# Optimization experiments

Hardware: AMD Instinct MI355X
Metric: run time of the kernel (lower is better)

Reference implementation:

```python
import jax, jax.numpy as jnp
import numpy as np

PRE_NMS_TOP_N = 1024
POST_NMS_TOP_N = 256
NMS_THRESH = 0.7
MIN_SIZE = 4.0
SCORE_THRESH = 0.1
BASE_SIZE = 1024.0
SCALE = 0.25            # feature stride = 1/SCALE = 4
IMG_H, IMG_W = 1024.0, 1024.0
NEG_INF = -1e30
CAP = 8                 # max vertices of 4-gon intersect 4-gon


def setup_inputs() -> dict:
    key = jax.random.key(0)
    k1, k2 = jax.random.split(key)
    N, A, H, W = 2, 1, 256, 256
    objectness = jax.random.normal(k1, (N, A, H, W), dtype=jnp.float32)
    box_regression = jax.random.uniform(k2, (N, A * 5, H, W), dtype=jnp.float32) * 0.05
    return {"objectness": objectness, "box_regression": box_regression}


def eastbox2rbox(reg, H, W):
    # reg: (H*W, 5) -> rotated boxes (H*W, 5) in xywha (angle in degrees)
    jy, jx = jnp.meshgrid(jnp.arange(H, dtype=reg.dtype), jnp.arange(W, dtype=reg.dtype), indexing="ij")
    cx0 = (jx / SCALE).reshape(-1)
    cy0 = (jy / SCALE).reshape(-1)
    t = reg[:, 0] * BASE_SIZE
    r = reg[:, 1] * BASE_SIZE
    b = reg[:, 2] * BASE_SIZE
    l = reg[:, 3] * BASE_SIZE
    ang = (reg[:, 4] - 0.5) * 90.0
    w = l + r
    h = t + b
    xc = cx0 + 0.5 * (r - l)
    yc = cy0 + 0.5 * (b - t)
    return jnp.stack([xc, yc, w, h, ang], axis=-1)


def rbox_corners(box):
    # box: (5,) xywha -> (4,2) CCW corners
    th = box[4] * (jnp.pi / 180.0)
    c, s = jnp.cos(th), jnp.sin(th)
    dx = jnp.array([-0.5, 0.5, 0.5, -0.5], box.dtype) * box[2]
    dy = jnp.array([-0.5, -0.5, 0.5, 0.5], box.dtype) * box[3]
    return jnp.stack([box[0] + dx * c - dy * s, box[1] + dx * s + dy * c], axis=-1)


def clip_halfplane(poly, n, p1, p2):
    # Sutherland-Hodgman clip of a convex polygon (CAP,2) with n valid verts
    # against the half-plane left of directed edge p1->p2.
    M = poly.shape[0]
    idx = jnp.arange(M)
    valid = idx < n
    nxt = poly[jnp.where(idx + 1 < n, idx + 1, 0)]
    e = p2 - p1
    d_cur = e[0] * (poly[:, 1] - p1[1]) - e[1] * (poly[:, 0] - p1[0])
    d_nxt = e[0] * (nxt[:, 1] - p1[1]) - e[1] * (nxt[:, 0] - p1[0])
    in_cur = d_cur >= 0.0
    in_nxt = d_nxt >= 0.0
    denom = d_cur - d_nxt
    safe = jnp.where(jnp.abs(denom) > 1e-9, denom, 1.0)
    t = d_cur / safe
    inter = poly + t[:, None] * (nxt - poly)
    emit_cur = in_cur & valid
    emit_int = (in_cur != in_nxt) & valid
    pts = jnp.stack([poly, inter], axis=1).reshape(2 * M, 2)
    flags = jnp.stack([emit_cur, emit_int], axis=1).reshape(2 * M)
    pos = jnp.where(flags, jnp.cumsum(flags) - 1, M)  # M = dropped
    out = jnp.zeros((M, 2), poly.dtype).at[pos].set(jnp.where(flags[:, None], pts, 0.0), mode="drop")
    return out, jnp.sum(flags)


def intersect_area(pa, pb):
    # area of convex intersection of two 4-gons (each (4,2), CCW)
    poly = jnp.zeros((CAP, 2), pa.dtype).at[:4].set(pa)
    n = jnp.asarray(4, jnp.int32)
    for k in range(4):
        poly, n = clip_halfplane(poly, n, pb[k], pb[(k + 1) % 4])
    idx = jnp.arange(CAP)
    valid = idx < n
    nxt = poly[jnp.where(idx + 1 < n, idx + 1, 0)]
    cr = poly[:, 0] * nxt[:, 1] - nxt[:, 0] * poly[:, 1]
    area = 0.5 * jnp.abs(jnp.sum(jnp.where(valid, cr, 0.0)))
    return jnp.where(n >= 3, area, 0.0)


def riou(a, b):
    inter = intersect_area(rbox_corners(a), rbox_corners(b))
    union = a[2] * a[3] + b[2] * b[3] - inter
    return inter / jnp.maximum(union, 1e-9)


def greedy_nms(iou_mat, valid, thresh):
    K = valid.shape[0]
    ar = jnp.arange(K)

    def body(i, state):
        keep, sup = state
        is_keep = valid[i] & jnp.logical_not(sup[i])
        keep = keep.at[i].set(is_keep)
        sup = sup | (is_keep & (iou_mat[i] > thresh) & (ar > i))
        return keep, sup

    keep, _ = jax.lax.fori_loop(0, K, body, (jnp.zeros(K, bool), jnp.zeros(K, bool)))
    return keep


def process_image(obj, reg):
    A, H, W = obj.shape
    scores = obj.transpose(1, 2, 0).reshape(-1)       # (H*W*A,)
    reg5 = reg[:5].transpose(1, 2, 0).reshape(-1, 5)  # (H*W, 5)
    rboxes = eastbox2rbox(reg5, H, W)
    top_scores, top_idx = jax.lax.top_k(scores, PRE_NMS_TOP_N)
    boxes = rboxes[top_idx]
    valid = top_scores > SCORE_THRESH                 # eval-mode score thresh (masked, not dropped)
    # clip_to_image: clamp rotated-box centers into the image
    boxes = boxes.at[:, 0].set(jnp.clip(boxes[:, 0], 0.0, IMG_W - 1.0))
    boxes = boxes.at[:, 1].set(jnp.clip(boxes[:, 1], 0.0, IMG_H - 1.0))
    # remove_small_boxes
    valid = valid & (boxes[:, 2] >= MIN_SIZE) & (boxes[:, 3] >= MIN_SIZE)
    # full rotated IoU matrix, row-by-row to bound memory
    iou_mat = jax.lax.map(lambda a: jax.vmap(lambda b: riou(a, b))(boxes), boxes)
    keep = greedy_nms(iou_mat, valid, NMS_THRESH)
    sel = jnp.where(keep, top_scores, NEG_INF)
    fin_scores, fin_idx = jax.lax.top_k(sel, POST_NMS_TOP_N)
    fin_boxes = boxes[fin_idx]
    fin_valid = keep[fin_idx]
    out = jnp.concatenate([fin_boxes, fin_scores[:, None]], axis=-1)  # (post, 6) = xywha + score
    return jnp.where(fin_valid[:, None], out, 0.0)


def reference(objectness, box_regression):
    return jax.vmap(process_image)(objectness, box_regression)
```

## Files before the change

kernel.cpp:

```cpp
#include <hip/hip_runtime.h>
#include <hip/hip_bf16.h>

#define N_IMG 2
#define HW 65536
#define PRE 1024
#define POST 256
#define NBIN 4096
#define SORTN 4096
#define PAIRCAP 131072
#define NMS_THR 0.7f
#define SCORE_T 0.1f
#define MIN_SZ 4.0f

__device__ __forceinline__ unsigned int fkey(float f) {
    unsigned int u = __float_as_uint(f);
    return u ^ ((u & 0x80000000u) ? 0xFFFFFFFFu : 0x80000000u);
}
__device__ __forceinline__ float unfkey(unsigned int k) {
    unsigned int u = (k & 0x80000000u) ? (k ^ 0x80000000u) : ~k;
    return __uint_as_float(u);
}
__device__ __forceinline__ unsigned long long readlane64(unsigned long long v, int l) {
    unsigned int lo = (unsigned int)__builtin_amdgcn_readlane((int)(unsigned int)v, l);
    unsigned int hi = (unsigned int)__builtin_amdgcn_readlane((int)(unsigned int)(v >> 32), l);
    return ((unsigned long long)hi << 32) | (unsigned long long)lo;
}

__global__ void k_init(unsigned long long* masks, unsigned int* hist, unsigned int* cnts) {
    int t = blockIdx.x * blockDim.x + threadIdx.x;
    if (t < N_IMG * PRE * 16) masks[t] = 0ULL;
    if (t < N_IMG * NBIN) hist[t] = 0u;
    if (t < 8) cnts[t] = 0u;
}

__global__ __launch_bounds__(1024) void k_hista(const float* __restrict__ obj,
                                                unsigned int* hist) {
    __shared__ unsigned int lh[NBIN];
    int img = blockIdx.x >> 3;
    int seg = blockIdx.x & 7;
    for (int i = threadIdx.x; i < NBIN; i += 1024) lh[i] = 0u;
    __syncthreads();
    const float4* o4 = (const float4*)(obj + (size_t)img * HW);
    int base = seg * 2048;
#pragma unroll
    for (int k = 0; k < 2; ++k) {
        float4 v = o4[base + threadIdx.x + k * 1024];
        atomicAdd(&lh[fkey(v.x) >> 20], 1u);
        atomicAdd(&lh[fkey(v.y) >> 20], 1u);
        atomicAdd(&lh[fkey(v.z) >> 20], 1u);
        atomicAdd(&lh[fkey(v.w) >> 20], 1u);
    }
    __syncthreads();
    for (int i = threadIdx.x; i < NBIN; i += 1024) {
        unsigned int c = lh[i];
        if (c) atomicAdd(&hist[img * NBIN + i], c);
    }
}

__global__ void k_findbin(const unsigned int* __restrict__ hist, unsigned int* selB) {
    __shared__ unsigned int lh[NBIN];
    __shared__ unsigned int chunk[256];
    int img = blockIdx.x;
    int t = threadIdx.x;
    unsigned int s = 0;
    for (int k = 0; k < 16; ++k) {
        unsigned int v = hist[img * NBIN + t * 16 + k];
        lh[t * 16 + k] = v;
        s += v;
    }
    chunk[t] = s;
    __syncthreads();
    if (t == 0) {
        unsigned int run = 0;
        int c;
        for (c = 255; c >= 0; --c) {
            if (run + chunk[c] >= PRE) break;
            run += chunk[c];
        }
        unsigned int B = 0;
        for (int b = c * 16 + 15; b >= c * 16; --b) {
            if (run + lh[b] >= PRE) { B = (unsigned int)b; break; }
            run += lh[b];
        }
        selB[img] = B;
    }
}

__global__ __launch_bounds__(256) void k_compact(const float* __restrict__ obj,
                                                 const unsigned int* __restrict__ selB,
                                                 unsigned int* cnts, unsigned long long* cbuf) {
    __shared__ unsigned long long lbuf[1024];
    __shared__ unsigned int lcnt, lbase;
    int t = blockIdx.x * 256 + threadIdx.x;
    const float4* o4 = (const float4*)obj;
#pragma unroll
    for (int k = 0; k < 2; ++k) {
        if (threadIdx.x == 0) lcnt = 0;
        __syncthreads();
        int p = t + k * 16384;
        int img = p >> 14;
        unsigned int B = selB[img];
        float4 v = o4[p];
        float vs[4] = {v.x, v.y, v.z, v.w};
#pragma unroll
        for (int c = 0; c < 4; ++c) {
            unsigned int key = fkey(vs[c]);
            if ((key >> 20) >= B) {
                unsigned int i = (unsigned int)((p & 16383) * 4 + c);
                unsigned int pos = atomicAdd(&lcnt, 1u);
                lbuf[pos] = ((unsigned long long)key << 32) |
                            (unsigned long long)(0xFFFFFFFFu - i);
            }
        }
        __syncthreads();
        if (threadIdx.x == 0) lbase = atomicAdd(&cnts[img], lcnt);
        __syncthreads();
        unsigned int n = lcnt, base = lbase;
        for (unsigned int q = threadIdx.x; q < n; q += 256) {
            unsigned int gp = base + q;
            if (gp < SORTN) cbuf[img * SORTN + gp] = lbuf[q];
        }
        __syncthreads();
    }
}

__global__ __launch_bounds__(256) void k_rank(const unsigned int* __restrict__ cnts,
                                              const unsigned long long* __restrict__ cbuf,
                                              unsigned long long* sorted) {
    __shared__ unsigned long long keys[SORTN];
    int img = blockIdx.x >> 4;
    int slice = blockIdx.x & 15;
    unsigned int M = cnts[img]; if (M > SORTN) M = SORTN;
    for (unsigned int i = threadIdx.x; i < M; i += 256) keys[i] = cbuf[img * SORTN + i];
    __syncthreads();
    unsigned int cid = (unsigned int)slice * 256 + threadIdx.x;
    if (cid < M) {
        unsigned long long c = keys[cid];
        unsigned int r = 0;
        for (unsigned int j = 0; j < M; ++j) r += (keys[j] > c) ? 1u : 0u;
        if (r < PRE) sorted[img * PRE + r] = c;
    }
}

__global__ __launch_bounds__(128) void k_decode(const unsigned long long* __restrict__ sorted,
                                                const float* __restrict__ boxreg,
                                                float* boxes, float* corn, float4* circ,
                                                unsigned long long* vmask, float* tscr) {
    int g = blockIdx.x * 128 + threadIdx.x;
    int img = g >> 10;
    int t = g & 1023;
    unsigned long long v = sorted[g];
    unsigned int key = (unsigned int)(v >> 32);
    unsigned int idx = (0xFFFFFFFFu - (unsigned int)(v & 0xFFFFFFFFULL)) & 0xFFFFu;
    float sc = unfkey(key);
    int h = (int)(idx >> 8);
    int w = (int)(idx & 255u);
    const float* rg = boxreg + (size_t)img * 5 * HW;
    float t_ = rg[0 * HW + idx] * 1024.0f;
    float rr = rg[1 * HW + idx] * 1024.0f;
    float bb = rg[2 * HW + idx] * 1024.0f;
    float ll = rg[3 * HW + idx] * 1024.0f;
    float ang = (rg[4 * HW + idx] - 0.5f) * 90.0f;
    float wd = ll + rr;
    float ht = t_ + bb;
    float xc = (float)w * 4.0f + 0.5f * (rr - ll);
    float yc = (float)h * 4.0f + 0.5f * (bb - t_);
    xc = fminf(fmaxf(xc, 0.0f), 1023.0f);
    yc = fminf(fmaxf(yc, 0.0f), 1023.0f);
    bool valid = (sc > SCORE_T) && (wd >= MIN_SZ) && (ht >= MIN_SZ);

    float* bx = boxes + (size_t)g * 5;
    bx[0] = xc; bx[1] = yc; bx[2] = wd; bx[3] = ht; bx[4] = ang;
    tscr[g] = sc;

    float th = ang * (float)(3.14159265358979323846 / 180.0);
    float c = cosf(th), s = sinf(th);
    const float dxs[4] = {-0.5f, 0.5f, 0.5f, -0.5f};
    const float dys[4] = {-0.5f, -0.5f, 0.5f, 0.5f};
    float* cr = corn + (size_t)g * 8;
#pragma unroll
    for (int k = 0; k < 4; ++k) {
        float dx = dxs[k] * wd, dy = dys[k] * ht;
        cr[2 * k]     = xc + dx * c - dy * s;
        cr[2 * k + 1] = yc + dx * s + dy * c;
    }
    circ[g] = make_float4(xc, yc, 0.5f * sqrtf(wd * wd + ht * ht) + 0.01f, wd * ht);

    unsigned long long bal = __ballot(valid ? 1 : 0);
    if ((t & 63) == 0) vmask[img * 16 + (t >> 6)] = bal;
}

__global__ __launch_bounds__(256) void k_pairs(const float4* __restrict__ circ,
                                               unsigned int* cnts, unsigned int* pairs) {
    __shared__ unsigned int lbuf[1024];
    __shared__ unsigned int lcnt, lbase;
    if (threadIdx.x == 0) lcnt = 0;
    __syncthreads();
    int t0 = blockIdx.x * 256 + threadIdx.x;
#pragma unroll
    for (int k = 0; k < 16; ++k) {
        int p = t0 + k * 131072;
        int img = p >> 20;
        int r = p & 1048575;
        int i = r >> 10, j = r & 1023;
        if (j > i) {
            float4 a = circ[img * PRE + i];
            float4 b = circ[img * PRE + j];
            float dx = b.x - a.x, dy = b.y - a.y, rr = a.z + b.z;
            if (dx * dx + dy * dy <= rr * rr) {
                unsigned int pr = ((unsigned int)img << 20) | ((unsigned int)i << 10) | (unsigned int)j;
                unsigned int pos = atomicAdd(&lcnt, 1u);
                if (pos < 1024) lbuf[pos] = pr;
                else {
                    unsigned int gp = atomicAdd(&cnts[2], 1u);
                    if (gp < PAIRCAP) pairs[gp] = pr;
                }
            }
        }
    }
    __syncthreads();
    unsigned int n = lcnt; if (n > 1024) n = 1024;
    if (threadIdx.x == 0) lbase = atomicAdd(&cnts[2], n);
    __syncthreads();
    unsigned int base = lbase;
    for (unsigned int q = threadIdx.x; q < n; q += 256) {
        unsigned int gp = base + q;
        if (gp < PAIRCAP) pairs[gp] = lbuf[q];
    }
}

__global__ __launch_bounds__(256) void k_clip(const unsigned int* __restrict__ cnts,
                                              const unsigned int* __restrict__ pairs,
                                              const float* __restrict__ corn,
                                              const float4* __restrict__ circ,
                                              unsigned long long* masks) {
    __shared__ float SPX[8][256], SPY[8][256], SQX[8][256], SQY[8][256];
    int tid = threadIdx.x;
    unsigned int total = cnts[2]; if (total > PAIRCAP) total = PAIRCAP;
    for (unsigned int p = blockIdx.x * 256 + tid; p < total; p += 128 * 256) {
        unsigned int pr = pairs[p];
        int img = (int)(pr >> 20);
        int i = (int)((pr >> 10) & 1023);
        int j = (int)(pr & 1023);
        int ra = img * PRE + i, rb = img * PRE + j;
        const float4* ca = (const float4*)(corn + (size_t)ra * 8);
        float4 a0 = ca[0], a1 = ca[1];
        const float4* cb = (const float4*)(corn + (size_t)rb * 8);
        float4 b0 = cb[0], b1 = cb[1];
        float cbx[4] = {b0.x, b0.z, b1.x, b1.z};
        float cby[4] = {b0.y, b0.w, b1.y, b1.w};
        SPX[0][tid] = a0.x; SPY[0][tid] = a0.y;
        SPX[1][tid] = a0.z; SPY[1][tid] = a0.w;
        SPX[2][tid] = a1.x; SPY[2][tid] = a1.y;
        SPX[3][tid] = a1.z; SPY[3][tid] = a1.w;
        int n = 4;
#pragma unroll
        for (int e = 0; e < 4; ++e) {
            float (*PX)[256] = (e & 1) ? SQX : SPX;
            float (*PY)[256] = (e & 1) ? SQY : SPY;
            float (*QX)[256] = (e & 1) ? SPX : SQX;
            float (*QY)[256] = (e & 1) ? SPY : SQY;
            float p1x = cbx[e], p1y = cby[e];
            int e2 = (e + 1) & 3;
            float ex = cbx[e2] - p1x, ey = cby[e2] - p1y;
            int m = 0;
            for (int k = 0; k < n; ++k) {
                int kn = (k + 1 < n) ? k + 1 : 0;
                float cx_ = PX[k][tid], cy_ = PY[k][tid];
                float nx_ = PX[kn][tid], ny_ = PY[kn][tid];
                float dc = ex * (cy_ - p1y) - ey * (cx_ - p1x);
                float dn = ex * (ny_ - p1y) - ey * (nx_ - p1x);
                bool ic = dc >= 0.0f;
                bool inx = dn >= 0.0f;
                if (ic && m < 8) { QX[m][tid] = cx_; QY[m][tid] = cy_; ++m; }
                if ((ic != inx) && m < 8) {
                    float den = dc - dn;
                    float safe = (fabsf(den) > 1e-9f) ? den : 1.0f;
                    float tt = dc / safe;
                    QX[m][tid] = cx_ + tt * (nx_ - cx_);
                    QY[m][tid] = cy_ + tt * (ny_ - cy_);
                    ++m;
                }
            }
            n = m;
        }
        float inter = 0.0f;
        if (n >= 3) {
            float s = 0.0f;
            for (int k = 0; k < n; ++k) {
                int kn = (k + 1 < n) ? k + 1 : 0;
                s += SPX[k][tid] * SPY[kn][tid] - SPX[kn][tid] * SPY[k][tid];
            }
            inter = 0.5f * fabsf(s);
        }
        float uni = circ[ra].w + circ[rb].w - inter;
        float iou = inter / fmaxf(uni, 1e-9f);
        if (iou > NMS_THR)
            atomicOr(&masks[(size_t)ra * 16 + (j >> 6)], 1ULL << (j & 63));
    }
}

__global__ __launch_bounds__(1024) void k_nms_out(const unsigned long long* __restrict__ masks,
                                                  const unsigned long long* __restrict__ vmask,
                                                  const float* __restrict__ boxes,
                                                  const float* __restrict__ tscr,
                                                  float* __restrict__ out) {
    __shared__ unsigned long long lm[PRE * 16];
    __shared__ unsigned short keptIdx[POST];
    __shared__ int sTotal;
    int img = blockIdx.x;
    int t = threadIdx.x;
    const unsigned long long* mbase = masks + (size_t)img * PRE * 16;
    {
        const ulonglong2* src = (const ulonglong2*)mbase;
        ulonglong2* dst = (ulonglong2*)lm;
#pragma unroll
        for (int k = 0; k < 8; ++k) dst[t + k * 1024] = src[t + k * 1024];
    }
    __syncthreads();

    if (t < 64) {
        int lane = t;
        int lw = lane & 15;
        unsigned long long vmw = vmask[img * 16 + lw];
        unsigned long long supw = 0ULL;
        int cnt = 0;
        for (int b = 0; b < 16 && cnt < POST; ++b) {
            unsigned long long avail = readlane64(vmw, b) & ~readlane64(supw, b);
            while (avail && cnt < POST) {
                unsigned long long a = avail;
                int d0 = __ffsll((long long)a) - 1; a &= a - 1;
                int d1 = a ? __ffsll((long long)a) - 1 : 64; a &= a - 1;
                int d2 = a ? __ffsll((long long)a) - 1 : 64; a &= a - 1;
                int d3 = a ? __ffsll((long long)a) - 1 : 64; a &= a - 1;
                int r0 = b * 64 + d0;
                int r1 = b * 64 + (d1 & 63);
                int r2 = b * 64 + (d2 & 63);
                int r3 = b * 64 + (d3 & 63);
                unsigned long long w0 = lm[r0 * 16 + lw];
                unsigned long long w1 = lm[r1 * 16 + lw];
                unsigned long long w2 = lm[r2 * 16 + lw];
                unsigned long long w3 = lm[r3 * 16 + lw];
                unsigned long long sb = readlane64(w0, b);
                supw |= w0;
                if (lane == 0) keptIdx[cnt] = (unsigned short)r0;
                ++cnt;
                if (d1 < 64 && cnt < POST && !((sb >> d1) & 1ULL)) {
                    sb |= readlane64(w1, b); supw |= w1;
                    if (lane == 0) keptIdx[cnt] = (unsigned short)r1;
                    ++cnt;
                }
                if (d2 < 64 && cnt < POST && !((sb >> d2) & 1ULL)) {
                    sb |= readlane64(w2, b); supw |= w2;
                    if (lane == 0) keptIdx[cnt] = (unsigned short)r2;
                    ++cnt;
                }
                if (d3 < 64 && cnt < POST && !((sb >> d3) & 1ULL)) {
                    sb |= readlane64(w3, b); supw |= w3;
                    if (lane == 0) keptIdx[cnt] = (unsigned short)r3;
                    ++cnt;
                }
                avail = a & ~sb;
            }
        }
        if (lane == 0) sTotal = cnt;
    }
    __syncthreads();

    int total = sTotal;
    if (t < POST) {
        float v0 = 0.f, v1 = 0.f, v2 = 0.f, v3 = 0.f, v4 = 0.f, v5 = 0.f;
        if (t < total) {
            int i = keptIdx[t];
            const float* b = boxes + (size_t)(img * PRE + i) * 5;
            v0 = b[0]; v1 = b[1]; v2 = b[2]; v3 = b[3]; v4 = b[4];
            v5 = tscr[img * PRE + i];
        }
        float* o2 = out + (size_t)(img * POST + t) * 6;
        o2[0] = v0; o2[1] = v1; o2[2] = v2; o2[3] = v3; o2[4] = v4; o2[5] = v5;
    }
}

enum : size_t {
    OFF_BOX  = 0,
    OFF_CORN = 40960,
    OFF_CIRC = 106496,
    OFF_VMSK = 139264,
    OFF_TSCR = 139520,
    OFF_MASK = 147712,
    OFF_HIST = 409856,
    OFF_CNTS = 442624,
    OFF_SELB = 442656,
    OFF_CBUF = 442672,
    OFF_SORT = 508208,
    OFF_PAIR = 524592,
};

extern "C" void kernel_launch(void* const* d_in, const int* in_sizes, int n_in,
                              void* d_out, int out_size, void* d_ws, size_t ws_size,
                              hipStream_t stream) {
    const float* obj = (const float*)d_in[0];
    const float* boxreg = (const float*)d_in[1];
    float* out = (float*)d_out;

    char* w = (char*)d_ws;
    float* boxes = (float*)(w + OFF_BOX);
    float* corn = (float*)(w + OFF_CORN);
    float4* circ = (float4*)(w + OFF_CIRC);
    unsigned long long* vmask = (unsigned long long*)(w + OFF_VMSK);
    float* tscr = (float*)(w + OFF_TSCR);
    unsigned long long* masks = (unsigned long long*)(w + OFF_MASK);
    unsigned int* hist = (unsigned int*)(w + OFF_HIST);
    unsigned int* cnts = (unsigned int*)(w + OFF_CNTS);
    unsigned int* selB = (unsigned int*)(w + OFF_SELB);
    unsigned long long* cbuf = (unsigned long long*)(w + OFF_CBUF);
    unsigned long long* sorted = (unsigned long long*)(w + OFF_SORT);
    unsigned int* pairs = (unsigned int*)(w + OFF_PAIR);

    k_init<<<160, 256, 0, stream>>>(masks, hist, cnts);
    k_hista<<<16, 1024, 0, stream>>>(obj, hist);
    k_findbin<<<N_IMG, 256, 0, stream>>>(hist, selB);
    k_compact<<<64, 256, 0, stream>>>(obj, selB, cnts, cbuf);
    k_rank<<<32, 256, 0, stream>>>(cnts, cbuf, sorted);
    k_decode<<<16, 128, 0, stream>>>(sorted, boxreg, boxes, corn, circ, vmask, tscr);
    k_pairs<<<512, 256, 0, stream>>>(circ, cnts, pairs);
    k_clip<<<128, 256, 0, stream>>>(cnts, pairs, corn, circ, masks);
    k_nms_out<<<N_IMG, 1024, 0, stream>>>(masks, vmask, boxes, tscr, out);
}
```

Measured before the change: 90.11 us.

## Fuse pipeline stages to cut kernel launches from nine to six

Folds the zeroing kernel into the histogram kernel and replaces global atomic histogram merging with per-block partial histograms summed in findbin. Rank and decode become one kernel, so the sorted buffer goes away, and pair detection is fused with polygon clipping through a shared-memory pair list flushed in batches. The valid mask is now built from a per-box array inside the NMS kernel. The goal is to remove launch overhead and global round trips for intermediate buffers. The cost is extra barriers in the pair/clip loop, and clip work is now spread over 512 blocks with uneven load.

```diff
diff --git a/kernel.cpp b/kernel.cpp
--- a/kernel.cpp
+++ b/kernel.cpp
@@ -7,7 +7,6 @@
 #define POST 256
 #define NBIN 4096
 #define SORTN 4096
-#define PAIRCAP 131072
 #define NMS_THR 0.7f
 #define SCORE_T 0.1f
 #define MIN_SZ 4.0f
@@ -26,19 +25,20 @@
     return ((unsigned long long)hi << 32) | (unsigned long long)lo;
 }
 
-__global__ void k_init(unsigned long long* masks, unsigned int* hist, unsigned int* cnts) {
-    int t = blockIdx.x * blockDim.x + threadIdx.x;
-    if (t < N_IMG * PRE * 16) masks[t] = 0ULL;
-    if (t < N_IMG * NBIN) hist[t] = 0u;
-    if (t < 8) cnts[t] = 0u;
-}
-
-__global__ __launch_bounds__(1024) void k_hista(const float* __restrict__ obj,
-                                                unsigned int* hist) {
+__global__ __launch_bounds__(1024) void k_front(const float* __restrict__ obj,
+                                                unsigned int* phist,
+                                                unsigned long long* masks,
+                                                unsigned int* cnts) {
     __shared__ unsigned int lh[NBIN];
     int img = blockIdx.x >> 3;
     int seg = blockIdx.x & 7;
     for (int i = threadIdx.x; i < NBIN; i += 1024) lh[i] = 0u;
+    {
+        unsigned long long* mz = masks + (size_t)blockIdx.x * 2048;
+        mz[threadIdx.x] = 0ULL;
+        mz[threadIdx.x + 1024] = 0ULL;
+    }
+    if (blockIdx.x == 0 && threadIdx.x < 8) cnts[threadIdx.x] = 0u;
     __syncthreads();
     const float4* o4 = (const float4*)(obj + (size_t)img * HW);
     int base = seg * 2048;
@@ -51,23 +51,25 @@
         atomicAdd(&lh[fkey(v.w) >> 20], 1u);
     }
     __syncthreads();
-    for (int i = threadIdx.x; i < NBIN; i += 1024) {
-        unsigned int c = lh[i];
-        if (c) atomicAdd(&hist[img * NBIN + i], c);
-    }
-}
-
-__global__ void k_findbin(const unsigned int* __restrict__ hist, unsigned int* selB) {
+    unsigned int* ph = phist + (size_t)blockIdx.x * NBIN;
+    for (int i = threadIdx.x; i < NBIN; i += 1024) ph[i] = lh[i];
+}
+
+__global__ void k_findbin(const unsigned int* __restrict__ phist, unsigned int* selB) {
     __shared__ unsigned int lh[NBIN];
     __shared__ unsigned int chunk[256];
     int img = blockIdx.x;
     int t = threadIdx.x;
+    for (int c = 0; c < 16; ++c) {
+        int b = c * 256 + t;
+        unsigned int v = 0;
+#pragma unroll
+        for (int q = 0; q < 8; ++q) v += phist[(size_t)(img * 8 + q) * NBIN + b];
+        lh[b] = v;
+    }
+    __syncthreads();
     unsigned int s = 0;
-    for (int k = 0; k < 16; ++k) {
-        unsigned int v = hist[img * NBIN + t * 16 + k];
-        lh[t * 16 + k] = v;
-        s += v;
-    }
+    for (int k = 0; k < 16; ++k) s += lh[t * 16 + k];
     chunk[t] = s;
     __syncthreads();
     if (t == 0) {
@@ -124,9 +126,11 @@
     }
 }
 
-__global__ __launch_bounds__(256) void k_rank(const unsigned int* __restrict__ cnts,
-                                              const unsigned long long* __restrict__ cbuf,
-                                              unsigned long long* sorted) {
+__global__ __launch_bounds__(256) void k_rankdec(const unsigned int* __restrict__ cnts,
+                                                 const unsigned long long* __restrict__ cbuf,
+                                                 const float* __restrict__ boxreg,
+                                                 float* boxes, float* corn, float4* circ,
+                                                 unsigned int* varr, float* tscr) {
     __shared__ unsigned long long keys[SORTN];
     int img = blockIdx.x >> 4;
     int slice = blockIdx.x & 15;
@@ -134,24 +138,15 @@
     for (unsigned int i = threadIdx.x; i < M; i += 256) keys[i] = cbuf[img * SORTN + i];
     __syncthreads();
     unsigned int cid = (unsigned int)slice * 256 + threadIdx.x;
-    if (cid < M) {
-        unsigned long long c = keys[cid];
-        unsigned int r = 0;
-        for (unsigned int j = 0; j < M; ++j) r += (keys[j] > c) ? 1u : 0u;
-        if (r < PRE) sorted[img * PRE + r] = c;
-    }
-}
-
-__global__ __launch_bounds__(128) void k_decode(const unsigned long long* __restrict__ sorted,
-                                                const float* __restrict__ boxreg,
-                                                float* boxes, float* corn, float4* circ,
-                                                unsigned long long* vmask, float* tscr) {
-    int g = blockIdx.x * 128 + threadIdx.x;
-    int img = g >> 10;
-    int t = g & 1023;
-    unsigned long long v = sorted[g];
-    unsigned int key = (unsigned int)(v >> 32);
-    unsigned int idx = (0xFFFFFFFFu - (unsigned int)(v & 0xFFFFFFFFULL)) & 0xFFFFu;
+    if (cid >= M) return;
+    unsigned long long cv = keys[cid];
+    unsigned int r = 0;
+    for (unsigned int j = 0; j < M; ++j) r += (keys[j] > cv) ? 1u : 0u;
+    if (r >= PRE) return;
+
+    int g = img * PRE + (int)r;
+    unsigned int key = (unsigned int)(cv >> 32);
+    unsigned int idx = (0xFFFFFFFFu - (unsigned int)(cv & 0xFFFFFFFFULL)) & 0xFFFFu;
     float sc = unfkey(key);
     int h = (int)(idx >> 8);
     int w = (int)(idx & 255u);
@@ -172,6 +167,7 @@
     float* bx = boxes + (size_t)g * 5;
     bx[0] = xc; bx[1] = yc; bx[2] = wd; bx[3] = ht; bx[4] = ang;
     tscr[g] = sc;
+    varr[g] = valid ? 1u : 0u;
 
     float th = ang * (float)(3.14159265358979323846 / 180.0);
     float c = cosf(th), s = sinf(th);
@@ -185,19 +181,18 @@
         cr[2 * k + 1] = yc + dx * s + dy * c;
     }
     circ[g] = make_float4(xc, yc, 0.5f * sqrtf(wd * wd + ht * ht) + 0.01f, wd * ht);
-
-    unsigned long long bal = __ballot(valid ? 1 : 0);
-    if ((t & 63) == 0) vmask[img * 16 + (t >> 6)] = bal;
-}
-
-__global__ __launch_bounds__(256) void k_pairs(const float4* __restrict__ circ,
-                                               unsigned int* cnts, unsigned int* pairs) {
-    __shared__ unsigned int lbuf[1024];
-    __shared__ unsigned int lcnt, lbase;
-    if (threadIdx.x == 0) lcnt = 0;
-    __syncthreads();
-    int t0 = blockIdx.x * 256 + threadIdx.x;
-#pragma unroll
+}
+
+__global__ __launch_bounds__(256) void k_pairclip(const float4* __restrict__ circ,
+                                                  const float* __restrict__ corn,
+                                                  unsigned long long* masks) {
+    __shared__ float SPX[8][256], SPY[8][256], SQX[8][256], SQY[8][256];
+    __shared__ unsigned int plist[1280];
+    __shared__ unsigned int pcnt;
+    int tid = threadIdx.x;
+    if (tid == 0) pcnt = 0;
+    __syncthreads();
+    int t0 = blockIdx.x * 256 + tid;
     for (int k = 0; k < 16; ++k) {
         int p = t0 + k * 131072;
         int img = p >> 20;
@@ -207,105 +202,88 @@
             float4 a = circ[img * PRE + i];
             float4 b = circ[img * PRE + j];
             float dx = b.x - a.x, dy = b.y - a.y, rr = a.z + b.z;
-            if (dx * dx + dy * dy <= rr * rr) {
-                unsigned int pr = ((unsigned int)img << 20) | ((unsigned int)i << 10) | (unsigned int)j;
-                unsigned int pos = atomicAdd(&lcnt, 1u);
-                if (pos < 1024) lbuf[pos] = pr;
-                else {
-                    unsigned int gp = atomicAdd(&cnts[2], 1u);
-                    if (gp < PAIRCAP) pairs[gp] = pr;
+            if (dx * dx + dy * dy <= rr * rr)
+                plist[atomicAdd(&pcnt, 1u)] =
+                    ((unsigned int)img << 20) | ((unsigned int)i << 10) | (unsigned int)j;
+        }
+        __syncthreads();
+        unsigned int n = pcnt;
+        if (n >= 1024 || k == 15) {
+            for (unsigned int q = tid; q < n; q += 256) {
+                unsigned int pr = plist[q];
+                int im = (int)(pr >> 20);
+                int bi = (int)((pr >> 10) & 1023);
+                int bj = (int)(pr & 1023);
+                int ra = im * PRE + bi, rb = im * PRE + bj;
+                const float4* ca = (const float4*)(corn + (size_t)ra * 8);
+                float4 a0 = ca[0], a1 = ca[1];
+                const float4* cb = (const float4*)(corn + (size_t)rb * 8);
+                float4 b0 = cb[0], b1 = cb[1];
+                float cbx[4] = {b0.x, b0.z, b1.x, b1.z};
+                float cby[4] = {b0.y, b0.w, b1.y, b1.w};
+                SPX[0][tid] = a0.x; SPY[0][tid] = a0.y;
+                SPX[1][tid] = a0.z; SPY[1][tid] = a0.w;
+                SPX[2][tid] = a1.x; SPY[2][tid] = a1.y;
+                SPX[3][tid] = a1.z; SPY[3][tid] = a1.w;
+                int n2 = 4;
+#pragma unroll
+                for (int e = 0; e < 4; ++e) {
+                    float (*PX)[256] = (e & 1) ? SQX : SPX;
+                    float (*PY)[256] = (e & 1) ? SQY : SPY;
+                    float (*QX)[256] = (e & 1) ? SPX : SQX;
+                    float (*QY)[256] = (e & 1) ? SPY : SQY;
+                    float p1x = cbx[e], p1y = cby[e];
+                    int e2 = (e + 1) & 3;
+                    float ex = cbx[e2] - p1x, ey = cby[e2] - p1y;
+                    int m = 0;
+                    for (int kk = 0; kk < n2; ++kk) {
+                        int kn = (kk + 1 < n2) ? kk + 1 : 0;
+                        float cx_ = PX[kk][tid], cy_ = PY[kk][tid];
+                        float nx_ = PX[kn][tid], ny_ = PY[kn][tid];
+                        float dc = ex * (cy_ - p1y) - ey * (cx_ - p1x);
+                        float dn = ex * (ny_ - p1y) - ey * (nx_ - p1x);
+                        bool ic = dc >= 0.0f;
+                        bool inx = dn >= 0.0f;
+                        if (ic && m < 8) { QX[m][tid] = cx_; QY[m][tid] = cy_; ++m; }
+                        if ((ic != inx) && m < 8) {
+                            float den = dc - dn;
+                            float safe = (fabsf(den) > 1e-9f) ? den : 1.0f;
+                            float tt = dc / safe;
+                            QX[m][tid] = cx_ + tt * (nx_ - cx_);
+                            QY[m][tid] = cy_ + tt * (ny_ - cy_);
+                            ++m;
+                        }
+                    }
+                    n2 = m;
                 }
+                float inter = 0.0f;
+                if (n2 >= 3) {
+                    float s = 0.0f;
+                    for (int kk = 0; kk < n2; ++kk) {
+                        int kn = (kk + 1 < n2) ? kk + 1 : 0;
+                        s += SPX[kk][tid] * SPY[kn][tid] - SPX[kn][tid] * SPY[kk][tid];
+                    }
+                    inter = 0.5f * fabsf(s);
+                }
+                float uni = circ[ra].w + circ[rb].w - inter;
+                float iou = inter / fmaxf(uni, 1e-9f);
+                if (iou > NMS_THR)
+                    atomicOr(&masks[(size_t)ra * 16 + (bj >> 6)], 1ULL << (bj & 63));
             }
-        }
-    }
-    __syncthreads();
-    unsigned int n = lcnt; if (n > 1024) n = 1024;
-    if (threadIdx.x == 0) lbase = atomicAdd(&cnts[2], n);
-    __syncthreads();
-    unsigned int base = lbase;
-    for (unsigned int q = threadIdx.x; q < n; q += 256) {
-        unsigned int gp = base + q;
-        if (gp < PAIRCAP) pairs[gp] = lbuf[q];
-    }
-}
-
-__global__ __launch_bounds__(256) void k_clip(const unsigned int* __restrict__ cnts,
-                                              const unsigned int* __restrict__ pairs,
-                                              const float* __restrict__ corn,
-                                              const float4* __restrict__ circ,
-                                              unsigned long long* masks) {
-    __shared__ float SPX[8][256], SPY[8][256], SQX[8][256], SQY[8][256];
-    int tid = threadIdx.x;
-    unsigned int total = cnts[2]; if (total > PAIRCAP) total = PAIRCAP;
-    for (unsigned int p = blockIdx.x * 256 + tid; p < total; p += 128 * 256) {
-        unsigned int pr = pairs[p];
-        int img = (int)(pr >> 20);
-        int i = (int)((pr >> 10) & 1023);
-        int j = (int)(pr & 1023);
-        int ra = img * PRE + i, rb = img * PRE + j;
-        const float4* ca = (const float4*)(corn + (size_t)ra * 8);
-        float4 a0 = ca[0], a1 = ca[1];
-        const float4* cb = (const float4*)(corn + (size_t)rb * 8);
-        float4 b0 = cb[0], b1 = cb[1];
-        float cbx[4] = {b0.x, b0.z, b1.x, b1.z};
-        float cby[4] = {b0.y, b0.w, b1.y, b1.w};
-        SPX[0][tid] = a0.x; SPY[0][tid] = a0.y;
-        SPX[1][tid] = a0.z; SPY[1][tid] = a0.w;
-        SPX[2][tid] = a1.x; SPY[2][tid] = a1.y;
-        SPX[3][tid] = a1.z; SPY[3][tid] = a1.w;
-        int n = 4;
-#pragma unroll
-        for (int e = 0; e < 4; ++e) {
-            float (*PX)[256] = (e & 1) ? SQX : SPX;
-            float (*PY)[256] = (e & 1) ? SQY : SPY;
-            float (*QX)[256] = (e & 1) ? SPX : SQX;
-            float (*QY)[256] = (e & 1) ? SPY : SQY;
-            float p1x = cbx[e], p1y = cby[e];
-            int e2 = (e + 1) & 3;
-            float ex = cbx[e2] - p1x, ey = cby[e2] - p1y;
-            int m = 0;
-            for (int k = 0; k < n; ++k) {
-                int kn = (k + 1 < n) ? k + 1 : 0;
-                float cx_ = PX[k][tid], cy_ = PY[k][tid];
-                float nx_ = PX[kn][tid], ny_ = PY[kn][tid];
-                float dc = ex * (cy_ - p1y) - ey * (cx_ - p1x);
-                float dn = ex * (ny_ - p1y) - ey * (nx_ - p1x);
-                bool ic = dc >= 0.0f;
-                bool inx = dn >= 0.0f;
-                if (ic && m < 8) { QX[m][tid] = cx_; QY[m][tid] = cy_; ++m; }
-                if ((ic != inx) && m < 8) {
-                    float den = dc - dn;
-                    float safe = (fabsf(den) > 1e-9f) ? den : 1.0f;
-                    float tt = dc / safe;
-                    QX[m][tid] = cx_ + tt * (nx_ - cx_);
-                    QY[m][tid] = cy_ + tt * (ny_ - cy_);
-                    ++m;
-                }
-            }
-            n = m;
-        }
-        float inter = 0.0f;
-        if (n >= 3) {
-            float s = 0.0f;
-            for (int k = 0; k < n; ++k) {
-                int kn = (k + 1 < n) ? k + 1 : 0;
-                s += SPX[k][tid] * SPY[kn][tid] - SPX[kn][tid] * SPY[k][tid];
-            }
-            inter = 0.5f * fabsf(s);
-        }
-        float uni = circ[ra].w + circ[rb].w - inter;
-        float iou = inter / fmaxf(uni, 1e-9f);
-        if (iou > NMS_THR)
-            atomicOr(&masks[(size_t)ra * 16 + (j >> 6)], 1ULL << (j & 63));
+            __syncthreads();
+            if (tid == 0) pcnt = 0;
+            __syncthreads();
+        }
     }
 }
 
 __global__ __launch_bounds__(1024) void k_nms_out(const unsigned long long* __restrict__ masks,
-                                                  const unsigned long long* __restrict__ vmask,
+                                                  const unsigned int* __restrict__ varr,
                                                   const float* __restrict__ boxes,
                                                   const float* __restrict__ tscr,
                                                   float* __restrict__ out) {
     __shared__ unsigned long long lm[PRE * 16];
+    __shared__ unsigned long long vmw_s[16];
     __shared__ unsigned short keptIdx[POST];
     __shared__ int sTotal;
     int img = blockIdx.x;
@@ -317,12 +295,16 @@
 #pragma unroll
         for (int k = 0; k < 8; ++k) dst[t + k * 1024] = src[t + k * 1024];
     }
+    {
+        unsigned long long bal = __ballot(varr[img * PRE + t] != 0u);
+        if ((t & 63) == 0) vmw_s[t >> 6] = bal;
+    }
     __syncthreads();
 
     if (t < 64) {
         int lane = t;
         int lw = lane & 15;
-        unsigned long long vmw = vmask[img * 16 + lw];
+        unsigned long long vmw = vmw_s[lw];
         unsigned long long supw = 0ULL;
         int cnt = 0;
         for (int b = 0; b < 16 && cnt < POST; ++b) {
@@ -382,18 +364,16 @@
 }
 
 enum : size_t {
-    OFF_BOX  = 0,
-    OFF_CORN = 40960,
-    OFF_CIRC = 106496,
-    OFF_VMSK = 139264,
-    OFF_TSCR = 139520,
-    OFF_MASK = 147712,
-    OFF_HIST = 409856,
-    OFF_CNTS = 442624,
-    OFF_SELB = 442656,
-    OFF_CBUF = 442672,
-    OFF_SORT = 508208,
-    OFF_PAIR = 524592,
+    OFF_BOX   = 0,
+    OFF_CORN  = 40960,
+    OFF_CIRC  = 106496,
+    OFF_VARR  = 139264,
+    OFF_TSCR  = 147456,
+    OFF_MASK  = 155648,
+    OFF_PHIST = 417792,
+    OFF_CNTS  = 679936,
+    OFF_SELB  = 679968,
+    OFF_CBUF  = 679984,
 };
 
 extern "C" void kernel_launch(void* const* d_in, const int* in_sizes, int n_in,
@@ -407,23 +387,18 @@
     float* boxes = (float*)(w + OFF_BOX);
     float* corn = (float*)(w + OFF_CORN);
     float4* circ = (float4*)(w + OFF_CIRC);
-    unsigned long long* vmask = (unsigned long long*)(w + OFF_VMSK);
+    unsigned int* varr = (unsigned int*)(w + OFF_VARR);
     float* tscr = (float*)(w + OFF_TSCR);
     unsigned long long* masks = (unsigned long long*)(w + OFF_MASK);
-    unsigned int* hist = (unsigned int*)(w + OFF_HIST);
+    unsigned int* phist = (unsigned int*)(w + OFF_PHIST);
     unsigned int* cnts = (unsigned int*)(w + OFF_CNTS);
     unsigned int* selB = (unsigned int*)(w + OFF_SELB);
     unsigned long long* cbuf = (unsigned long long*)(w + OFF_CBUF);
-    unsigned long long* sorted = (unsigned long long*)(w + OFF_SORT);
-    unsigned int* pairs = (unsigned int*)(w + OFF_PAIR);
-
-    k_init<<<160, 256, 0, stream>>>(masks, hist, cnts);
-    k_hista<<<16, 1024, 0, stream>>>(obj, hist);
-    k_findbin<<<N_IMG, 256, 0, stream>>>(hist, selB);
+
+    k_front<<<16, 1024, 0, stream>>>(obj, phist, masks, cnts);
+    k_findbin<<<N_IMG, 256, 0, stream>>>(phist, selB);
     k_compact<<<64, 256, 0, stream>>>(obj, selB, cnts, cbuf);
-    k_rank<<<32, 256, 0, stream>>>(cnts, cbuf, sorted);
-    k_decode<<<16, 128, 0, stream>>>(sorted, boxreg, boxes, corn, circ, vmask, tscr);
-    k_pairs<<<512, 256, 0, stream>>>(circ, cnts, pairs);
-    k_clip<<<128, 256, 0, stream>>>(cnts, pairs, corn, circ, masks);
-    k_nms_out<<<N_IMG, 1024, 0, stream>>>(masks, vmask, boxes, tscr, out);
-}
+    k_rankdec<<<32, 256, 0, stream>>>(cnts, cbuf, boxreg, boxes, corn, circ, varr, tscr);
+    k_pairclip<<<512, 256, 0, stream>>>(circ, corn, masks);
+    k_nms_out<<<N_IMG, 1024, 0, stream>>>(masks, varr, boxes, tscr, out);
+}
```

Measured after the change: 88.77 us. Within noise of the previous version (-1.5%).
